# Performance work log

Hardware: AMD Instinct MI355X
Metric: run time of the kernel (lower is better)

## Reference

```python
import jax, jax.numpy as jnp
import numpy as np

N_NODES = 50000
N_EDGES = 400000
NFEAT, NHID2, NHID3, NHID4, NCLASS = 500, 128, 128, 64, 40


def setup_inputs() -> dict:
    key = jax.random.key(0)
    ks = jax.random.split(key, 20)
    s = 0.05
    inp = {
        'x': jax.random.normal(ks[0], (N_NODES, NFEAT), jnp.float32),
        'src': jax.random.randint(ks[1], (4, N_EDGES), 0, N_NODES, jnp.int64 if jax.config.jax_enable_x64 else jnp.int32),
        'dst': jax.random.randint(ks[2], (4, N_EDGES), 0, N_NODES, jnp.int64 if jax.config.jax_enable_x64 else jnp.int32),
        'val': jax.random.uniform(ks[3], (4, N_EDGES), jnp.float32),
        'Wa': jax.random.normal(ks[4], (4, NFEAT, NHID2), jnp.float32) * s,
        'ba': jax.random.normal(ks[5], (4, NHID2), jnp.float32) * s,
        'Wb': jax.random.normal(ks[6], (4, NHID2, NHID3), jnp.float32) * s,
        'bb': jax.random.normal(ks[7], (4, NHID3), jnp.float32) * s,
        'Wc': jax.random.normal(ks[8], (4, NHID3, NHID4), jnp.float32) * s,
        'bc': jax.random.normal(ks[9], (4, NHID4), jnp.float32) * s,
        'dW': jax.random.normal(ks[10], (5, NHID4, NCLASS), jnp.float32) * s,
        'db': jax.random.normal(ks[11], (5, NCLASS), jnp.float32) * s,
        'e1W': jax.random.normal(ks[12], (4 * NHID4, NHID2), jnp.float32) * s,
        'e1b': jax.random.normal(ks[13], (NHID2,), jnp.float32) * s,
        'e2W': jax.random.normal(ks[14], (NHID2, NHID3), jnp.float32) * s,
        'e2b': jax.random.normal(ks[15], (NHID3,), jnp.float32) * s,
        'e3W': jax.random.normal(ks[16], (NHID3, NHID4), jnp.float32) * s,
        'e3b': jax.random.normal(ks[17], (NHID4,), jnp.float32) * s,
    }
    return inp


def _gcn(h, W, b, src, dst, val):
    # support = h @ W ; out = spmm(adj, support) + b  (Kipf GraphConvolution)
    support = h @ W                                   # [N, out]
    msg = support[src] * val[:, None]                 # [E, out] gather + scale
    return jax.ops.segment_sum(msg, dst, num_segments=N_NODES) + b


def reference(x, src, dst, val, Wa, ba, Wb, bb, Wc, bc, dW, db, e1W, e1b, e2W, e2b, e3W, e3b):
    # One GCN branch: relu(gcn) -> relu(gcn) -> gcn (dropout is inference no-op)
    def branch(Wa_i, ba_i, Wb_i, bb_i, Wc_i, bc_i, src_i, dst_i, val_i):
        h = jax.nn.relu(_gcn(x, Wa_i, ba_i, src_i, dst_i, val_i))
        h = jax.nn.relu(_gcn(h, Wb_i, bb_i, src_i, dst_i, val_i))
        return _gcn(h, Wc_i, bc_i, src_i, dst_i, val_i)  # pre-ReLU branch output

    xb = jax.vmap(branch)(Wa, ba, Wb, bb, Wc, bc, src, dst, val)  # [4, N, nhid4]

    # per-branch dense heads on relu(branch output)
    dense_out = jnp.einsum('knd,kdc->knc', jax.nn.relu(xb), dW[:4]) + db[:4, None, :]

    # ensemble MLP on concat(x1,x2,x3,x4)
    cat = jnp.transpose(xb, (1, 0, 2)).reshape(N_NODES, 4 * NHID4)
    e = jax.nn.relu(cat @ e1W + e1b)
    e = jax.nn.relu(e @ e2W + e2b)
    e = jax.nn.relu(e @ e3W + e3b)
    out5 = e @ dW[4] + db[4]

    return (dense_out[0], dense_out[1], dense_out[2], dense_out[3], out5)
```

## Files before the change

### kernel.cpp

```cpp
#include <hip/hip_runtime.h>
#include <stdint.h>

#define NN 50000
#define NE 400000
#define MPAD 50048
#define NF 500
#define KP 512

typedef __bf16 bf16;
typedef __bf16 bf16x8 __attribute__((ext_vector_type(8)));
typedef float  f32x4  __attribute__((ext_vector_type(4)));

__device__ __forceinline__ void gload16(const void* g, void* l) {
  __builtin_amdgcn_global_load_lds(
      (__attribute__((address_space(1))) void*)g,
      (__attribute__((address_space(3))) void*)l, 16, 0, 0);
}

__device__ __forceinline__ uint32_t packbf2(float a, float b) {
  union { bf16 h[2]; uint32_t u; } c;
  c.h[0] = (bf16)a; c.h[1] = (bf16)b;
  return c.u;
}

__global__ void k_conv_x(const float* __restrict__ x, bf16* __restrict__ xbf) {
  int idx = blockIdx.x * 256 + threadIdx.x;
  if (idx >= NN * KP) return;
  int n = idx >> 9, c = idx & (KP - 1);
  float v = (c < NF) ? x[n * NF + c] : 0.f;
  xbf[idx] = (bf16)v;
}

__global__ void k_conv_waT(const float* __restrict__ Wa, bf16* __restrict__ WaT) {
  int idx = blockIdx.x * 256 + threadIdx.x;
  if (idx >= 4 * 128 * KP) return;
  int b = idx >> 16;
  int r = idx & 65535;
  int n = r >> 9, k = r & 511;
  float v = (k < NF) ? Wa[(b * NF + k) * 128 + n] : 0.f;
  WaT[idx] = (bf16)v;
}

__global__ void k_conv_wT(const float* __restrict__ W, bf16* __restrict__ WT, int Kd, int Nd) {
  int idx = blockIdx.x * 256 + threadIdx.x;
  int tot = Kd * Nd;
  if (idx >= tot) return;
  int n = idx / Kd, k = idx - n * Kd;
  WT[(size_t)blockIdx.y * tot + idx] = (bf16)W[(size_t)blockIdx.y * tot + k * Nd + n];
}

__global__ void k_hist(const int* __restrict__ dst, int* __restrict__ counts) {
  int idx = blockIdx.x * 256 + threadIdx.x;
  if (idx >= 4 * NE) return;
  int b = idx / NE;
  atomicAdd(&counts[b * NN + dst[idx]], 1);
}

__global__ void __launch_bounds__(1024) k_scan(const int* __restrict__ counts, int* __restrict__ offs) {
  constexpr int CH = (NN + 1023) / 1024;
  int b = blockIdx.x;
  const int* c = counts + b * NN;
  int* o = offs + b * (NN + 1);
  __shared__ int part[1024];
  int t = threadIdx.x;
  int beg = t * CH, end = min(beg + CH, NN);
  int s = 0;
  for (int i = beg; i < end; ++i) s += c[i];
  part[t] = s;
  __syncthreads();
  for (int d = 1; d < 1024; d <<= 1) {
    int v = (t >= d) ? part[t - d] : 0;
    __syncthreads();
    part[t] += v;
    __syncthreads();
  }
  int run = t ? part[t - 1] : 0;
  for (int i = beg; i < end; ++i) { o[i] = run; run += c[i]; }
  if (t == 1023) o[NN] = part[1023];
}

__global__ void k_scatter(const int* __restrict__ src, const int* __restrict__ dst,
                          const float* __restrict__ val, const int* __restrict__ offs,
                          int* __restrict__ fill, int* __restrict__ csrc, float* __restrict__ cval) {
  int idx = blockIdx.x * 256 + threadIdx.x;
  if (idx >= 4 * NE) return;
  int b = idx / NE;
  int d = dst[idx];
  int pos = offs[b * (NN + 1) + d] + atomicAdd(&fill[b * NN + d], 1);
  csrc[b * NE + pos] = src[idx];
  cval[b * NE + pos] = val[idx];
}

template <int DIM>
__global__ void __launch_bounds__(256) k_spmm(
    const bf16* __restrict__ sup, const int* __restrict__ offs,
    const int* __restrict__ csrc, const float* __restrict__ cval,
    const float* __restrict__ bias, bf16* __restrict__ out,
    int ldOut, long long outBr, int relu) {
  constexpr int LPS = DIM / 8;
  constexpr int SLOTS = 64 / LPS;
  int b = blockIdx.z;
  int lane = threadIdx.x & 63;
  int slot = lane / LPS;
  int fl = lane % LPS;
  int n = blockIdx.x * 4 + (threadIdx.x >> 6);
  if (n >= NN) return;
  const int* o = offs + b * (NN + 1);
  int e0 = o[n], e1 = o[n + 1];
  const bf16* supb = sup + (size_t)b * MPAD * DIM;
  const int* sb = csrc + (size_t)b * NE;
  const float* vb = cval + (size_t)b * NE;

  float a[8];
#pragma unroll
  for (int j = 0; j < 8; ++j) a[j] = 0.f;

  int e = e0 + slot;
  for (; e + SLOTS < e1; e += 2 * SLOTS) {
    int s0 = sb[e];
    int s1 = sb[e + SLOTS];
    float v0 = vb[e];
    float v1 = vb[e + SLOTS];
    bf16x8 r0 = *(const bf16x8*)(supb + (size_t)s0 * DIM + fl * 8);
    bf16x8 r1 = *(const bf16x8*)(supb + (size_t)s1 * DIM + fl * 8);
#pragma unroll
    for (int j = 0; j < 8; ++j) a[j] = fmaf(v0, (float)r0[j], a[j]);
#pragma unroll
    for (int j = 0; j < 8; ++j) a[j] = fmaf(v1, (float)r1[j], a[j]);
  }
  if (e < e1) {
    int s0 = sb[e];
    float v0 = vb[e];
    bf16x8 r0 = *(const bf16x8*)(supb + (size_t)s0 * DIM + fl * 8);
#pragma unroll
    for (int j = 0; j < 8; ++j) a[j] = fmaf(v0, (float)r0[j], a[j]);
  }

#pragma unroll
  for (int m = LPS; m < 64; m <<= 1) {
#pragma unroll
    for (int j = 0; j < 8; ++j) a[j] += __shfl_xor(a[j], m, 64);
  }

  if (slot == 0) {
    const float* bi = bias + b * DIM + fl * 8;
#pragma unroll
    for (int j = 0; j < 8; ++j) {
      a[j] += bi[j];
      if (relu) a[j] = fmaxf(a[j], 0.f);
    }
    union { bf16 h[8]; uint4 u4; } pk;
#pragma unroll
    for (int j = 0; j < 8; ++j) pk.h[j] = (bf16)a[j];
    *(uint4*)(out + (size_t)b * outBr + (size_t)n * ldOut + fl * 8) = pk.u4;
  }
}

template <int BN, bool BR>
__global__ void __launch_bounds__(256) k_gemm(
    const bf16* __restrict__ A, const bf16* __restrict__ B, bf16* __restrict__ C,
    const float* __restrict__ bias, int K, int ldA, int ldC,
    size_t sA, size_t sB, size_t sC) {
  constexpr int WN = BN / 2;
  constexpr int NFR = WN / 16;
  constexpr int BL = BN / 32;
  __shared__ __align__(16) unsigned char sa[128 * 128];
  __shared__ __align__(16) unsigned char sb[BN * 128];
  int tid = threadIdx.x;
  int lane = tid & 63;
  int wid = tid >> 6;
  int wm = wid & 1, wn = wid >> 1;
  const bf16* Ab = A + sA * blockIdx.z;
  const bf16* Bb = B + sB * blockIdx.z;
  bf16* Cb = C + sC * blockIdx.z;
  int gm0 = blockIdx.x * 128;

  f32x4 acc[4][NFR];
#pragma unroll
  for (int i = 0; i < 4; ++i)
#pragma unroll
    for (int j = 0; j < NFR; ++j) acc[i][j] = (f32x4){0.f, 0.f, 0.f, 0.f};

  for (int kt = 0; kt < K; kt += 64) {
#pragma unroll
    for (int i = 0; i < 4; ++i) {
      int lb = (wid * 4 + i) * 1024 + lane * 16;
      int r = lb >> 7;
      int c = (lb >> 4) & 7;
      gload16(Ab + (size_t)(gm0 + r) * ldA + kt + ((c ^ (r & 7)) << 3),
              &sa[(wid * 4 + i) * 1024]);
    }
#pragma unroll
    for (int i = 0; i < BL; ++i) {
      int lb = (wid * BL + i) * 1024 + lane * 16;
      int r = lb >> 7;
      int c = (lb >> 4) & 7;
      gload16(Bb + (size_t)r * K + kt + ((c ^ (r & 7)) << 3),
              &sb[(wid * BL + i) * 1024]);
    }
    __syncthreads();
#pragma unroll
    for (int kk = 0; kk < 2; ++kk) {
      bf16x8 ar[4], br[NFR];
#pragma unroll
      for (int mi = 0; mi < 4; ++mi) {
        int r = wm * 64 + mi * 16 + (lane & 15);
        int c = (kk * 4 + (lane >> 4)) ^ (r & 7);
        ar[mi] = *(const bf16x8*)&sa[r * 128 + c * 16];
      }
#pragma unroll
      for (int ni = 0; ni < NFR; ++ni) {
        int r = wn * WN + ni * 16 + (lane & 15);
        int c = (kk * 4 + (lane >> 4)) ^ (r & 7);
        br[ni] = *(const bf16x8*)&sb[r * 128 + c * 16];
      }
#pragma unroll
      for (int mi = 0; mi < 4; ++mi)
#pragma unroll
        for (int ni = 0; ni < NFR; ++ni)
          acc[mi][ni] = __builtin_amdgcn_mfma_f32_16x16x32_bf16(br[ni], ar[mi], acc[mi][ni], 0, 0, 0);
    }
    __syncthreads();
  }

#pragma unroll
  for (int mi = 0; mi < 4; ++mi) {
    int m = gm0 + wm * 64 + mi * 16 + (lane & 15);
#pragma unroll
    for (int ni = 0; ni < NFR; ++ni) {
      int n0 = wn * WN + ni * 16 + ((lane >> 4) << 2);
      f32x4 v = acc[mi][ni];
      if (BR) {
        const f32x4 bv = *(const f32x4*)&bias[n0];
        v[0] = fmaxf(v[0] + bv[0], 0.f);
        v[1] = fmaxf(v[1] + bv[1], 0.f);
        v[2] = fmaxf(v[2] + bv[2], 0.f);
        v[3] = fmaxf(v[3] + bv[3], 0.f);
      }
      uint2 st;
      st.x = packbf2(v[0], v[1]);
      st.y = packbf2(v[2], v[3]);
      *(uint2*)(Cb + (size_t)m * ldC + n0) = st;
    }
  }
}

__global__ void k_head(const bf16* __restrict__ X, int ldX,
                       const float* __restrict__ W, const float* __restrict__ bias,
                       float* __restrict__ out) {
  int idx = blockIdx.x * 256 + threadIdx.x;
  if (idx >= NN * 40) return;
  int n = idx / 40, c = idx - n * 40;
  const bf16* xr = X + (size_t)n * ldX;
  float acc = bias[c];
#pragma unroll
  for (int d2 = 0; d2 < 32; ++d2) {
    union { uint32_t u; bf16 h[2]; } cv;
    cv.u = *(const uint32_t*)(xr + d2 * 2);
    acc = fmaf(fmaxf((float)cv.h[0], 0.f), W[(d2 * 2) * 40 + c], acc);
    acc = fmaf(fmaxf((float)cv.h[1], 0.f), W[(d2 * 2 + 1) * 40 + c], acc);
  }
  out[idx] = acc;
}

extern "C" void kernel_launch(void* const* d_in, const int* in_sizes, int n_in,
                              void* d_out, int out_size, void* d_ws, size_t ws_size,
                              hipStream_t stream) {
  (void)in_sizes; (void)n_in; (void)out_size; (void)ws_size;
  const float* x   = (const float*)d_in[0];
  const int*   src = (const int*)d_in[1];
  const int*   dst = (const int*)d_in[2];
  const float* val = (const float*)d_in[3];
  const float* Wa  = (const float*)d_in[4];
  const float* ba  = (const float*)d_in[5];
  const float* Wb  = (const float*)d_in[6];
  const float* bb  = (const float*)d_in[7];
  const float* Wc  = (const float*)d_in[8];
  const float* bc  = (const float*)d_in[9];
  const float* dW  = (const float*)d_in[10];
  const float* db  = (const float*)d_in[11];
  const float* e1W = (const float*)d_in[12];
  const float* e1b = (const float*)d_in[13];
  const float* e2W = (const float*)d_in[14];
  const float* e2b = (const float*)d_in[15];
  const float* e3W = (const float*)d_in[16];
  const float* e3b = (const float*)d_in[17];
  float* out = (float*)d_out;

  uint8_t* ws = (uint8_t*)d_ws;
  size_t off = 0;
  auto carve = [&](size_t sz) -> void* {
    void* p = ws + off;
    off = (off + sz + 255) & ~(size_t)255;
    return p;
  };

  bf16* xbf   = (bf16*)carve((size_t)MPAD * KP * 2);
  bf16* WaT   = (bf16*)carve((size_t)4 * 128 * KP * 2);
  bf16* WbT   = (bf16*)carve((size_t)4 * 128 * 128 * 2);
  bf16* WcT   = (bf16*)carve((size_t)4 * 64 * 128 * 2);
  bf16* e1WT  = (bf16*)carve((size_t)128 * 256 * 2);
  bf16* e2WT  = (bf16*)carve((size_t)128 * 128 * 2);
  bf16* e3WT  = (bf16*)carve((size_t)64 * 128 * 2);
  bf16* bufS  = (bf16*)carve((size_t)4 * MPAD * 128 * 2);
  bf16* bufH  = (bf16*)carve((size_t)4 * MPAD * 128 * 2);
  int*  counts= (int*)carve((size_t)4 * NN * 4);
  int*  fill  = (int*)carve((size_t)4 * NN * 4);
  int*  offs  = (int*)carve((size_t)4 * (NN + 1) * 4);
  int*  csrc  = (int*)carve((size_t)4 * NE * 4);
  float* cval = (float*)carve((size_t)4 * NE * 4);
  bf16* e1buf = xbf;
  bf16* e2buf = xbf + (size_t)MPAD * 128;
  bf16* e3buf = xbf + (size_t)2 * MPAD * 128;

  hipMemsetAsync(counts, 0, (size_t)2 * 4 * NN * 4, stream);

  k_conv_x  <<<(NN * KP + 255) / 256, 256, 0, stream>>>(x, xbf);
  k_conv_waT<<<(4 * 128 * KP + 255) / 256, 256, 0, stream>>>(Wa, WaT);
  k_conv_wT <<<dim3((128 * 128 + 255) / 256, 4), 256, 0, stream>>>(Wb, WbT, 128, 128);
  k_conv_wT <<<dim3((128 * 64 + 255) / 256, 4), 256, 0, stream>>>(Wc, WcT, 128, 64);
  k_conv_wT <<<dim3((256 * 128 + 255) / 256, 1), 256, 0, stream>>>(e1W, e1WT, 256, 128);
  k_conv_wT <<<dim3((128 * 128 + 255) / 256, 1), 256, 0, stream>>>(e2W, e2WT, 128, 128);
  k_conv_wT <<<dim3((128 * 64 + 255) / 256, 1), 256, 0, stream>>>(e3W, e3WT, 128, 64);

  k_hist   <<<(4 * NE + 255) / 256, 256, 0, stream>>>(dst, counts);
  k_scan   <<<4, 1024, 0, stream>>>(counts, offs);
  k_scatter<<<(4 * NE + 255) / 256, 256, 0, stream>>>(src, dst, val, offs, fill, csrc, cval);

  const dim3 gemmGrid4(MPAD / 128, 1, 4);
  const dim3 gemmGrid1(MPAD / 128, 1, 1);

  k_gemm<128, false><<<gemmGrid4, 256, 0, stream>>>(xbf, WaT, bufS, nullptr, KP, KP, 128,
                                                    0, (size_t)128 * KP, (size_t)MPAD * 128);
  k_spmm<128><<<dim3((NN + 3) / 4, 1, 4), 256, 0, stream>>>(bufS, offs, csrc, cval, ba, bufH,
                                                            128, (long long)MPAD * 128, 1);
  k_gemm<128, false><<<gemmGrid4, 256, 0, stream>>>(bufH, WbT, bufS, nullptr, 128, 128, 128,
                                                    (size_t)MPAD * 128, (size_t)128 * 128, (size_t)MPAD * 128);
  k_spmm<128><<<dim3((NN + 3) / 4, 1, 4), 256, 0, stream>>>(bufS, offs, csrc, cval, bb, bufH,
                                                            128, (long long)MPAD * 128, 1);
  k_gemm<64, false><<<gemmGrid4, 256, 0, stream>>>(bufH, WcT, bufS, nullptr, 128, 128, 64,
                                                   (size_t)MPAD * 128, (size_t)64 * 128, (size_t)MPAD * 64);
  k_spmm<64><<<dim3((NN + 3) / 4, 1, 4), 256, 0, stream>>>(bufS, offs, csrc, cval, bc, bufH,
                                                           256, 64, 0);
  for (int k = 0; k < 4; ++k)
    k_head<<<(NN * 40 + 255) / 256, 256, 0, stream>>>(bufH + k * 64, 256,
                                                      dW + (size_t)k * 64 * 40, db + k * 40,
                                                      out + (size_t)k * NN * 40);
  k_gemm<128, true><<<gemmGrid1, 256, 0, stream>>>(bufH, e1WT, e1buf, e1b, 256, 256, 128, 0, 0, 0);
  k_gemm<128, true><<<gemmGrid1, 256, 0, stream>>>(e1buf, e2WT, e2buf, e2b, 128, 128, 128, 0, 0, 0);
  k_gemm<64,  true><<<gemmGrid1, 256, 0, stream>>>(e2buf, e3WT, e3buf, e3b, 128, 128, 64, 0, 0, 0);
  k_head<<<(NN * 40 + 255) / 256, 256, 0, stream>>>(e3buf, 64, dW + (size_t)4 * 64 * 40, db + 4 * 40,
                                                    out + (size_t)4 * NN * 40);
}
```

Baseline: 956.7 us.

## Build CSR with two-level bucketed counting sort and packed edge records

Replaces the global-atomic histogram, single-block scan and atomic scatter with a two-pass bucketed sort. Edges are first binned into 256-node buckets using shared-memory histograms, then each bucket is sorted locally to produce offsets and packed (src,val) int2 records. The spmm kernel then reads one 8-byte record per edge instead of two separate arrays. The extra kernels and the staging buffer (aliased onto bufS) add passes over the edges in exchange for far fewer contended global atomics and a cheap scan.

```diff
diff --git a/kernel.cpp b/kernel.cpp
--- a/kernel.cpp
+++ b/kernel.cpp
@@ -6,6 +6,7 @@
 #define MPAD 50048
 #define NF 500
 #define KP 512
+#define NBK 196
 
 typedef __bf16 bf16;
 typedef __bf16 bf16x8 __attribute__((ext_vector_type(8)));
@@ -49,52 +50,130 @@
   WT[(size_t)blockIdx.y * tot + idx] = (bf16)W[(size_t)blockIdx.y * tot + k * Nd + n];
 }
 
-__global__ void k_hist(const int* __restrict__ dst, int* __restrict__ counts) {
-  int idx = blockIdx.x * 256 + threadIdx.x;
-  if (idx >= 4 * NE) return;
-  int b = idx / NE;
-  atomicAdd(&counts[b * NN + dst[idx]], 1);
-}
-
-__global__ void __launch_bounds__(1024) k_scan(const int* __restrict__ counts, int* __restrict__ offs) {
-  constexpr int CH = (NN + 1023) / 1024;
-  int b = blockIdx.x;
-  const int* c = counts + b * NN;
-  int* o = offs + b * (NN + 1);
-  __shared__ int part[1024];
+__global__ void __launch_bounds__(256) k_bhist(const int* __restrict__ dst, int* __restrict__ bcnt) {
+  __shared__ int h[256];
   int t = threadIdx.x;
-  int beg = t * CH, end = min(beg + CH, NN);
-  int s = 0;
-  for (int i = beg; i < end; ++i) s += c[i];
-  part[t] = s;
-  __syncthreads();
-  for (int d = 1; d < 1024; d <<= 1) {
-    int v = (t >= d) ? part[t - d] : 0;
-    __syncthreads();
-    part[t] += v;
-    __syncthreads();
-  }
-  int run = t ? part[t - 1] : 0;
-  for (int i = beg; i < end; ++i) { o[i] = run; run += c[i]; }
-  if (t == 1023) o[NN] = part[1023];
-}
-
-__global__ void k_scatter(const int* __restrict__ src, const int* __restrict__ dst,
-                          const float* __restrict__ val, const int* __restrict__ offs,
-                          int* __restrict__ fill, int* __restrict__ csrc, float* __restrict__ cval) {
-  int idx = blockIdx.x * 256 + threadIdx.x;
-  if (idx >= 4 * NE) return;
-  int b = idx / NE;
-  int d = dst[idx];
-  int pos = offs[b * (NN + 1) + d] + atomicAdd(&fill[b * NN + d], 1);
-  csrc[b * NE + pos] = src[idx];
-  cval[b * NE + pos] = val[idx];
+  int z = blockIdx.z;
+  h[t] = 0;
+  __syncthreads();
+  int e0 = blockIdx.x * 4096;
+#pragma unroll
+  for (int i = 0; i < 16; ++i) {
+    int e = e0 + i * 256 + t;
+    if (e < NE) atomicAdd(&h[dst[z * NE + e] >> 8], 1);
+  }
+  __syncthreads();
+  if (t < NBK && h[t] > 0) atomicAdd(&bcnt[z * NBK + t], h[t]);
+}
+
+__global__ void __launch_bounds__(256) k_bscan(const int* __restrict__ bcnt,
+                                               int* __restrict__ bases, int* __restrict__ gfill,
+                                               int* __restrict__ offs) {
+  __shared__ int ps[256];
+  int t = threadIdx.x;
+  for (int z = 0; z < 4; ++z) {
+    int c = (t < NBK) ? bcnt[z * NBK + t] : 0;
+    ps[t] = c;
+    __syncthreads();
+    for (int d = 1; d < 256; d <<= 1) {
+      int v = (t >= d) ? ps[t - d] : 0;
+      __syncthreads();
+      ps[t] += v;
+      __syncthreads();
+    }
+    if (t < NBK) {
+      int ex = ps[t] - c;
+      bases[z * (NBK + 1) + t] = ex;
+      gfill[z * NBK + t] = ex;
+      if (t == NBK - 1) bases[z * (NBK + 1) + NBK] = ps[t];
+    }
+    if (t == 0) offs[z * (NN + 1) + NN] = NE;
+    __syncthreads();
+  }
+}
+
+__global__ void __launch_bounds__(256) k_bin(const int* __restrict__ src, const int* __restrict__ dst,
+                                             const float* __restrict__ val, int* __restrict__ gfill,
+                                             int4* __restrict__ staging) {
+  __shared__ int h[256];
+  __shared__ int f2[256];
+  __shared__ int base[256];
+  int t = threadIdx.x;
+  int z = blockIdx.z;
+  h[t] = 0; f2[t] = 0;
+  __syncthreads();
+  int e0 = blockIdx.x * 4096;
+  int se[16], sd[16], sv[16];
+#pragma unroll
+  for (int i = 0; i < 16; ++i) {
+    int e = e0 + i * 256 + t;
+    sd[i] = -1;
+    if (e < NE) {
+      sd[i] = dst[z * NE + e];
+      se[i] = src[z * NE + e];
+      sv[i] = ((const int*)val)[z * NE + e];
+      atomicAdd(&h[sd[i] >> 8], 1);
+    }
+  }
+  __syncthreads();
+  if (t < NBK) {
+    int c = h[t];
+    base[t] = c ? atomicAdd(&gfill[z * NBK + t], c) : 0;
+  }
+  __syncthreads();
+#pragma unroll
+  for (int i = 0; i < 16; ++i) {
+    if (sd[i] >= 0) {
+      int bkt = sd[i] >> 8;
+      int loc = atomicAdd(&f2[bkt], 1);
+      staging[(size_t)z * NE + base[bkt] + loc] = make_int4(se[i], sd[i], sv[i], 0);
+    }
+  }
+}
+
+__global__ void __launch_bounds__(256) k_fine(const int4* __restrict__ staging,
+                                              const int* __restrict__ bases,
+                                              int* __restrict__ offs, int2* __restrict__ edata) {
+  __shared__ int cnts[256];
+  __shared__ int ps[256];
+  __shared__ int exl[256];
+  __shared__ int fl[256];
+  int t = threadIdx.x;
+  int z = blockIdx.z;
+  int bkt = blockIdx.x;
+  int base = bases[z * (NBK + 1) + bkt];
+  int endp = bases[z * (NBK + 1) + bkt + 1];
+  cnts[t] = 0; fl[t] = 0;
+  __syncthreads();
+  for (int e = base + t; e < endp; e += 256) {
+    int dl = staging[(size_t)z * NE + e].y & 255;
+    atomicAdd(&cnts[dl], 1);
+  }
+  __syncthreads();
+  ps[t] = cnts[t];
+  __syncthreads();
+  for (int d = 1; d < 256; d <<= 1) {
+    int v = (t >= d) ? ps[t - d] : 0;
+    __syncthreads();
+    ps[t] += v;
+    __syncthreads();
+  }
+  exl[t] = ps[t] - cnts[t];
+  int node0 = bkt * 256;
+  if (node0 + t < NN) offs[z * (NN + 1) + node0 + t] = base + exl[t];
+  __syncthreads();
+  for (int e = base + t; e < endp; e += 256) {
+    int4 g = staging[(size_t)z * NE + e];
+    int dl = g.y & 255;
+    int r = atomicAdd(&fl[dl], 1);
+    edata[(size_t)z * NE + base + exl[dl] + r] = make_int2(g.x, g.z);
+  }
 }
 
 template <int DIM>
 __global__ void __launch_bounds__(256) k_spmm(
     const bf16* __restrict__ sup, const int* __restrict__ offs,
-    const int* __restrict__ csrc, const float* __restrict__ cval,
+    const int2* __restrict__ edata,
     const float* __restrict__ bias, bf16* __restrict__ out,
     int ldOut, long long outBr, int relu) {
   constexpr int LPS = DIM / 8;
@@ -108,8 +187,7 @@
   const int* o = offs + b * (NN + 1);
   int e0 = o[n], e1 = o[n + 1];
   const bf16* supb = sup + (size_t)b * MPAD * DIM;
-  const int* sb = csrc + (size_t)b * NE;
-  const float* vb = cval + (size_t)b * NE;
+  const int2* eb = edata + (size_t)b * NE;
 
   float a[8];
 #pragma unroll
@@ -117,21 +195,21 @@
 
   int e = e0 + slot;
   for (; e + SLOTS < e1; e += 2 * SLOTS) {
-    int s0 = sb[e];
-    int s1 = sb[e + SLOTS];
-    float v0 = vb[e];
-    float v1 = vb[e + SLOTS];
-    bf16x8 r0 = *(const bf16x8*)(supb + (size_t)s0 * DIM + fl * 8);
-    bf16x8 r1 = *(const bf16x8*)(supb + (size_t)s1 * DIM + fl * 8);
+    int2 p0 = eb[e];
+    int2 p1 = eb[e + SLOTS];
+    float v0 = __int_as_float(p0.y);
+    float v1 = __int_as_float(p1.y);
+    bf16x8 r0 = *(const bf16x8*)(supb + (size_t)p0.x * DIM + fl * 8);
+    bf16x8 r1 = *(const bf16x8*)(supb + (size_t)p1.x * DIM + fl * 8);
 #pragma unroll
     for (int j = 0; j < 8; ++j) a[j] = fmaf(v0, (float)r0[j], a[j]);
 #pragma unroll
     for (int j = 0; j < 8; ++j) a[j] = fmaf(v1, (float)r1[j], a[j]);
   }
   if (e < e1) {
-    int s0 = sb[e];
-    float v0 = vb[e];
-    bf16x8 r0 = *(const bf16x8*)(supb + (size_t)s0 * DIM + fl * 8);
+    int2 p0 = eb[e];
+    float v0 = __int_as_float(p0.y);
+    bf16x8 r0 = *(const bf16x8*)(supb + (size_t)p0.x * DIM + fl * 8);
 #pragma unroll
     for (int j = 0; j < 8; ++j) a[j] = fmaf(v0, (float)r0[j], a[j]);
   }
@@ -304,16 +382,17 @@
   bf16* e3WT  = (bf16*)carve((size_t)64 * 128 * 2);
   bf16* bufS  = (bf16*)carve((size_t)4 * MPAD * 128 * 2);
   bf16* bufH  = (bf16*)carve((size_t)4 * MPAD * 128 * 2);
-  int*  counts= (int*)carve((size_t)4 * NN * 4);
-  int*  fill  = (int*)carve((size_t)4 * NN * 4);
+  int*  bcnt  = (int*)carve((size_t)4 * NBK * 4);
+  int*  gfill = (int*)carve((size_t)4 * NBK * 4);
+  int*  bases = (int*)carve((size_t)4 * (NBK + 1) * 4);
   int*  offs  = (int*)carve((size_t)4 * (NN + 1) * 4);
-  int*  csrc  = (int*)carve((size_t)4 * NE * 4);
-  float* cval = (float*)carve((size_t)4 * NE * 4);
+  int2* edata = (int2*)carve((size_t)4 * NE * 8);
+  int4* staging = (int4*)bufS;
   bf16* e1buf = xbf;
   bf16* e2buf = xbf + (size_t)MPAD * 128;
   bf16* e3buf = xbf + (size_t)2 * MPAD * 128;
 
-  hipMemsetAsync(counts, 0, (size_t)2 * 4 * NN * 4, stream);
+  hipMemsetAsync(bcnt, 0, (size_t)4 * NBK * 4, stream);
 
   k_conv_x  <<<(NN * KP + 255) / 256, 256, 0, stream>>>(x, xbf);
   k_conv_waT<<<(4 * 128 * KP + 255) / 256, 256, 0, stream>>>(Wa, WaT);
@@ -323,24 +402,26 @@
   k_conv_wT <<<dim3((128 * 128 + 255) / 256, 1), 256, 0, stream>>>(e2W, e2WT, 128, 128);
   k_conv_wT <<<dim3((128 * 64 + 255) / 256, 1), 256, 0, stream>>>(e3W, e3WT, 128, 64);
 
-  k_hist   <<<(4 * NE + 255) / 256, 256, 0, stream>>>(dst, counts);
-  k_scan   <<<4, 1024, 0, stream>>>(counts, offs);
-  k_scatter<<<(4 * NE + 255) / 256, 256, 0, stream>>>(src, dst, val, offs, fill, csrc, cval);
+  const int EB = (NE + 4095) / 4096;
+  k_bhist<<<dim3(EB, 1, 4), 256, 0, stream>>>(dst, bcnt);
+  k_bscan<<<1, 256, 0, stream>>>(bcnt, bases, gfill, offs);
+  k_bin  <<<dim3(EB, 1, 4), 256, 0, stream>>>(src, dst, val, gfill, staging);
+  k_fine <<<dim3(NBK, 1, 4), 256, 0, stream>>>(staging, bases, offs, edata);
 
   const dim3 gemmGrid4(MPAD / 128, 1, 4);
   const dim3 gemmGrid1(MPAD / 128, 1, 1);
 
   k_gemm<128, false><<<gemmGrid4, 256, 0, stream>>>(xbf, WaT, bufS, nullptr, KP, KP, 128,
                                                     0, (size_t)128 * KP, (size_t)MPAD * 128);
-  k_spmm<128><<<dim3((NN + 3) / 4, 1, 4), 256, 0, stream>>>(bufS, offs, csrc, cval, ba, bufH,
+  k_spmm<128><<<dim3((NN + 3) / 4, 1, 4), 256, 0, stream>>>(bufS, offs, edata, ba, bufH,
                                                             128, (long long)MPAD * 128, 1);
   k_gemm<128, false><<<gemmGrid4, 256, 0, stream>>>(bufH, WbT, bufS, nullptr, 128, 128, 128,
                                                     (size_t)MPAD * 128, (size_t)128 * 128, (size_t)MPAD * 128);
-  k_spmm<128><<<dim3((NN + 3) / 4, 1, 4), 256, 0, stream>>>(bufS, offs, csrc, cval, bb, bufH,
+  k_spmm<128><<<dim3((NN + 3) / 4, 1, 4), 256, 0, stream>>>(bufS, offs, edata, bb, bufH,
                                                             128, (long long)MPAD * 128, 1);
   k_gemm<64, false><<<gemmGrid4, 256, 0, stream>>>(bufH, WcT, bufS, nullptr, 128, 128, 64,
                                                    (size_t)MPAD * 128, (size_t)64 * 128, (size_t)MPAD * 64);
-  k_spmm<64><<<dim3((NN + 3) / 4, 1, 4), 256, 0, stream>>>(bufS, offs, csrc, cval, bc, bufH,
+  k_spmm<64><<<dim3((NN + 3) / 4, 1, 4), 256, 0, stream>>>(bufS, offs, edata, bc, bufH,
                                                            256, 64, 0);
   for (int k = 0; k < 4; ++k)
     k_head<<<(NN * 40 + 255) / 256, 256, 0, stream>>>(bufH + k * 64, 256,
```

After: 776.1 us. 1.23x faster.
